# Optimization experiments

Hardware: AMD Instinct MI355X
Metric: run time of the kernel (lower is better)

Reference implementation:

```python
import jax, jax.numpy as jnp
import numpy as np

B, S, D, H = 8, 128, 256, 8
T = S + 1
HD = D // H  # head_dim = 32
GAMMA = 1.0
NEG_INF = -1e9
LN_EPS = 1e-5


def setup_inputs() -> dict:
    key = jax.random.key(0)
    ks = jax.random.split(key, 16)
    sc = 0.05
    return {
        "desc_embeddings": jax.random.normal(ks[0], (B, S, D), jnp.float32),
        "name_value_embeddings": jax.random.normal(ks[1], (B, T, D), jnp.float32),
        "prior_Q": jax.random.uniform(ks[2], (B, H, S, S), jnp.float32),
        "Wq": jax.random.normal(ks[3], (D, D), jnp.float32) * sc,
        "bq": jnp.zeros((D,), jnp.float32),
        "Wk": jax.random.normal(ks[4], (D, D), jnp.float32) * sc,
        "bk": jnp.zeros((D,), jnp.float32),
        "Wv": jax.random.normal(ks[5], (D, D), jnp.float32) * sc,
        "bv": jnp.zeros((D,), jnp.float32),
        "wa": jax.random.normal(ks[6], (3 * HD,), jnp.float32) * sc,  # attn_proj weight (out=1)
        "ba": jnp.zeros((), jnp.float32),
        "We1": jax.random.normal(ks[7], (2 * D, D), jnp.float32) * sc,
        "be1": jnp.zeros((D,), jnp.float32),
        "ln_g": jnp.ones((D,), jnp.float32),
        "ln_b": jnp.zeros((D,), jnp.float32),
        "We2": jax.random.normal(ks[8], (D, D), jnp.float32) * sc,
        "be2": jnp.zeros((D,), jnp.float32),
    }


def _layer_norm(x, g, b):
    mu = jnp.mean(x, axis=-1, keepdims=True)
    var = jnp.mean(jnp.square(x - mu), axis=-1, keepdims=True)
    return (x - mu) * jax.lax.rsqrt(var + LN_EPS) * g + b


def _heads(x, W, b):  # [B,T,D] -> [B,H,T,HD]
    return (x @ W + b).reshape(B, T, H, HD).transpose(0, 2, 1, 3)


def reference(desc_embeddings, name_value_embeddings, prior_Q,
              Wq, bq, Wk, bk, Wv, bv, wa, ba,
              We1, be1, ln_g, ln_b, We2, be2):
    # structural adjacency (same for every batch element): CLS->Var on, Var->CLS off,
    # Var-Var fully connected without self-loops
    adj = jnp.zeros((T, T), jnp.float32)
    adj = adj.at[1:, 1:].set(1.0 - jnp.eye(S, dtype=jnp.float32))
    adj = adj.at[0, 1:].set(1.0)

    q = _heads(name_value_embeddings, Wq, bq)  # [B,H,T,HD]
    k = _heads(name_value_embeddings, Wk, bk)
    v = _heads(name_value_embeddings, Wv, bv)

    # edge attributes: pairwise concat of desc embeddings, CLS rows/cols use [desc,desc]
    desc = desc_embeddings
    var_edge = jnp.concatenate([
        jnp.broadcast_to(desc[:, :, None, :], (B, S, S, D)),
        jnp.broadcast_to(desc[:, None, :, :], (B, S, S, D)),
    ], axis=-1)  # [B,S,S,2D]
    cls_edge = jnp.concatenate([desc, desc], axis=-1)  # [B,S,2D]
    edge = jnp.zeros((B, T, T, 2 * D), jnp.float32)
    edge = edge.at[:, 1:, 1:].set(var_edge)
    edge = edge.at[:, 0, 1:].set(cls_edge)
    edge = edge.at[:, 1:, 0].set(cls_edge)

    # edge_update MLP: Linear(2D->D) -> LayerNorm -> ReLU -> Linear(D->D)
    h = jax.nn.relu(_layer_norm(edge @ We1 + be1, ln_g, ln_b)) @ We2 + be2  # [B,T,T,D]
    # split into heads, mask by adjacency: [B,H,T,T,HD]
    edge_h = h.reshape(B, T, T, H, HD).transpose(0, 3, 1, 2, 4)
    edge_h = edge_h * adj[None, None, :, :, None]

    # gat_v1 + attn_proj(cat[q_i, k_j, e_ij]) is linear -> decompose to avoid
    # materializing the [B,H,T,T,3*HD] concat
    wa_q, wa_k, wa_e = wa[:HD], wa[HD:2 * HD], wa[2 * HD:]
    logits = (jnp.einsum('bhid,d->bhi', q, wa_q)[:, :, :, None]
              + jnp.einsum('bhjd,d->bhj', k, wa_k)[:, :, None, :]
              + jnp.einsum('bhijd,d->bhij', edge_h, wa_e)
              + ba)  # [B,H,T,T]

    # prior_Q logit-bias injection on Var-Var block
    eps = 1e-6
    p = jnp.clip(prior_Q, eps, 1.0 - eps)
    bias = (jnp.log(p) - jnp.log(1.0 - p)) * GAMMA  # [B,H,S,S]
    logits = logits.at[:, :, 1:, 1:].add(bias)

    # structural mask as pre-softmax -inf
    logits = logits + (adj == 0).astype(logits.dtype)[None, None] * NEG_INF

    attn = jax.nn.softmax(logits, axis=-1)  # [B,H,T,T]
    ctx = jnp.einsum('bhij,bhjd->bhid', attn, v)  # [B,H,T,HD]
    basis_outputs = ctx.transpose(0, 2, 1, 3)  # [B,T,H,HD]
    return basis_outputs, attn
```

## Files before the change

kernel.cpp:

```cpp
#include <hip/hip_runtime.h>
#include <math.h>

#define B 8
#define S 128
#define D 256
#define H 8
#define T 129
#define HD 32
#define NEG_INF -1000000000.0f
#define LN_EPS 1e-5f

__global__ __launch_bounds__(256) void gemm_all(
    const float* __restrict__ nv, const float* __restrict__ desc,
    const float* __restrict__ Wq, const float* __restrict__ bq,
    const float* __restrict__ Wk, const float* __restrict__ bk,
    const float* __restrict__ Wv, const float* __restrict__ bv,
    const float* __restrict__ We1, const float* __restrict__ be1,
    const float* __restrict__ We2, const float* __restrict__ be2,
    const float* __restrict__ wa,
    float* __restrict__ v, float* __restrict__ U, float* __restrict__ V,
    float* __restrict__ qdkd, float* __restrict__ W2aT, float* __restrict__ econst)
{
    const int blk = blockIdx.x;
    const int tid = threadIdx.x;

    __shared__ float xs[16][260];
    __shared__ float wq_s[256 * 16];
    __shared__ float bq_s[16];

    if (blk < 193) {
        const float* X; const float* W; const float* bias; float* out; int rows; int r0;
        if (blk < 65)       { X = nv;   W = Wv;        bias = bv;      out = v; rows = B*T; r0 = blk * 16; }
        else if (blk < 129) { X = desc; W = We1;       bias = be1;     out = U; rows = B*S; r0 = (blk - 65) * 16; }
        else                { X = desc; W = We1 + D*D; bias = nullptr; out = V; rows = B*S; r0 = (blk - 129) * 16; }

        for (int t = tid; t < 16 * 256; t += 256) {
            const int r = t >> 8, c = t & 255, rr = r0 + r;
            xs[r][c] = (rr < rows) ? X[rr * D + c] : 0.f;
        }
        __syncthreads();

        const int c  = tid & 127;
        const int rg = (tid >> 7) * 8;

        float acc[8][2];
        #pragma unroll
        for (int r = 0; r < 8; ++r) { acc[r][0] = 0.f; acc[r][1] = 0.f; }

        float wA[8], wB[8], nA[8], nB[8];
        #pragma unroll
        for (int q = 0; q < 8; ++q) { wA[q] = W[q*D + c]; wB[q] = W[q*D + c + 128]; }

        for (int kk = 0; kk < 256; kk += 8) {
            const int kn = kk + 8;
            if (kn < 256) {
                #pragma unroll
                for (int q = 0; q < 8; ++q) {
                    nA[q] = W[(kn + q)*D + c];
                    nB[q] = W[(kn + q)*D + c + 128];
                }
            }
            #pragma unroll
            for (int qh = 0; qh < 8; qh += 4) {
                #pragma unroll
                for (int r = 0; r < 8; ++r) {
                    const float4 x = *(const float4*)&xs[rg + r][kk + qh];
                    acc[r][0] = fmaf(x.x, wA[qh+0], acc[r][0]);
                    acc[r][0] = fmaf(x.y, wA[qh+1], acc[r][0]);
                    acc[r][0] = fmaf(x.z, wA[qh+2], acc[r][0]);
                    acc[r][0] = fmaf(x.w, wA[qh+3], acc[r][0]);
                    acc[r][1] = fmaf(x.x, wB[qh+0], acc[r][1]);
                    acc[r][1] = fmaf(x.y, wB[qh+1], acc[r][1]);
                    acc[r][1] = fmaf(x.z, wB[qh+2], acc[r][1]);
                    acc[r][1] = fmaf(x.w, wB[qh+3], acc[r][1]);
                }
            }
            if (kn < 256) {
                #pragma unroll
                for (int q = 0; q < 8; ++q) { wA[q] = nA[q]; wB[q] = nB[q]; }
            }
        }

        const float b0 = bias ? bias[c]       : 0.f;
        const float b1 = bias ? bias[c + 128] : 0.f;
        #pragma unroll
        for (int r = 0; r < 8; ++r) {
            const int rr = r0 + rg + r;
            if (rr < rows) {
                out[rr * D + c]       = acc[r][0] + b0;
                out[rr * D + c + 128] = acc[r][1] + b1;
            }
        }
    } else if (blk < 258) {
        const int r0 = (blk - 193) * 16;

        for (int t = tid; t < 4096; t += 256) {
            const int k = t >> 4, cc = t & 15;
            const float* Wsrc = (cc < 8) ? Wq : Wk;
            const float* wap  = (cc < 8) ? wa : wa + HD;
            const int h = cc & 7;
            float s = 0.f;
            #pragma unroll
            for (int d = 0; d < HD; ++d) s = fmaf(Wsrc[k*D + h*HD + d], wap[d], s);
            wq_s[t] = s;
        }
        if (tid < 16) {
            const float* bsrc = (tid < 8) ? bq : bk;
            const float* wap  = (tid < 8) ? wa : wa + HD;
            const int h = tid & 7;
            float s = 0.f;
            #pragma unroll
            for (int d = 0; d < HD; ++d) s = fmaf(bsrc[h*HD + d], wap[d], s);
            bq_s[tid] = s;
        }
        for (int t = tid; t < 16 * 256; t += 256) {
            const int r = t >> 8, c = t & 255, rr = r0 + r;
            xs[r][c] = (rr < B*T) ? nv[rr * D + c] : 0.f;
        }
        __syncthreads();

        const int r = tid >> 4, cc = tid & 15;
        float acc = 0.f;
        for (int kk = 0; kk < 256; kk += 4) {
            const float4 x = *(const float4*)&xs[r][kk];
            acc = fmaf(x.x, wq_s[(kk+0)*16 + cc], acc);
            acc = fmaf(x.y, wq_s[(kk+1)*16 + cc], acc);
            acc = fmaf(x.z, wq_s[(kk+2)*16 + cc], acc);
            acc = fmaf(x.w, wq_s[(kk+3)*16 + cc], acc);
        }
        const int rr = r0 + r;
        if (rr < B*T) qdkd[rr * 16 + cc] = acc + bq_s[cc];
    } else {
        for (int t = tid; t < 2048; t += 256) {
            const int h = t >> 8, c = t & 255;
            float s = 0.f;
            #pragma unroll
            for (int d = 0; d < HD; ++d) s = fmaf(We2[c*D + h*HD + d], wa[2*HD + d], s);
            W2aT[h*D + c] = s;
        }
        if (tid < 8) {
            float s = 0.f;
            #pragma unroll
            for (int d = 0; d < HD; ++d) s = fmaf(be2[tid*HD + d], wa[2*HD + d], s);
            econst[tid] = s;
        }
    }
}

__global__ __launch_bounds__(512) void edge_attn(
    const float* __restrict__ U, const float* __restrict__ V,
    const float* __restrict__ W2aT, const float* __restrict__ econst,
    const float* __restrict__ ln_g, const float* __restrict__ ln_b,
    const float* __restrict__ qdkd, const float* __restrict__ prior,
    const float* __restrict__ v, const float* __restrict__ ba,
    float* __restrict__ out_basis, float* __restrict__ out_attn)
{
    const int bid = blockIdx.x;
    const int b = bid / T, i = bid % T;
    const int tid = threadIdx.x, lane = tid & 63, wid = tid >> 6;
    const int c0 = lane * 4;

    __shared__ float escl[H][132];
    __shared__ float pat[H][132];

    const float4 g4 = *(const float4*)(ln_g + c0);
    const float4 b4 = *(const float4*)(ln_b + c0);
    float4 w[H];
    #pragma unroll
    for (int h = 0; h < H; ++h) w[h] = *(const float4*)(W2aT + h*D + c0);
    float4 u4i = make_float4(0.f, 0.f, 0.f, 0.f);
    if (i >= 1) u4i = *(const float4*)(U + (b*S + (i-1))*D + c0);

    const int hmap = 4*(lane&1) + 2*((lane>>1)&1) + ((lane>>2)&1);
    const float ecl = (lane < 8) ? econst[hmap] : 0.f;

    const int j0 = 1 + wid * 16;
    for (int jj = 0; jj < 16; ++jj) {
        const int j = j0 + jj;
        if (i >= 1 && j == i) continue;

        const float4 v4 = *(const float4*)(V + (b*S + (j-1))*D + c0);
        float4 u4;
        if (i == 0) u4 = *(const float4*)(U + (b*S + (j-1))*D + c0);
        else        u4 = u4i;

        const float y0 = u4.x + v4.x, y1 = u4.y + v4.y;
        const float y2 = u4.z + v4.z, y3 = u4.w + v4.w;

        float s1 = y0 + y1 + y2 + y3;
        float s2 = fmaf(y0, y0, fmaf(y1, y1, fmaf(y2, y2, y3 * y3)));
        #pragma unroll
        for (int m = 32; m >= 1; m >>= 1) {
            s1 += __shfl_xor(s1, m);
            s2 += __shfl_xor(s2, m);
        }
        const float mu  = s1 * (1.f / D);
        const float var = s2 * (1.f / D) - mu * mu;
        const float rs  = rsqrtf(var + LN_EPS);

        const float t0 = fmaxf((y0 - mu) * rs * g4.x + b4.x, 0.f);
        const float t1 = fmaxf((y1 - mu) * rs * g4.y + b4.y, 0.f);
        const float t2 = fmaxf((y2 - mu) * rs * g4.z + b4.z, 0.f);
        const float t3 = fmaxf((y3 - mu) * rs * g4.w + b4.w, 0.f);

        float ph[H];
        #pragma unroll
        for (int h = 0; h < H; ++h)
            ph[h] = fmaf(t0, w[h].x, fmaf(t1, w[h].y, fmaf(t2, w[h].z, t3 * w[h].w)));

        {
            const bool hi = (lane & 1);
            float k0 = hi ? ph[4] : ph[0], d0 = hi ? ph[0] : ph[4];
            float k1 = hi ? ph[5] : ph[1], d1 = hi ? ph[1] : ph[5];
            float k2 = hi ? ph[6] : ph[2], d2 = hi ? ph[2] : ph[6];
            float k3 = hi ? ph[7] : ph[3], d3 = hi ? ph[3] : ph[7];
            ph[0] = k0 + __shfl_xor(d0, 1);
            ph[1] = k1 + __shfl_xor(d1, 1);
            ph[2] = k2 + __shfl_xor(d2, 1);
            ph[3] = k3 + __shfl_xor(d3, 1);
        }
        {
            const bool hi = (lane & 2);
            float k0 = hi ? ph[2] : ph[0], d0 = hi ? ph[0] : ph[2];
            float k1 = hi ? ph[3] : ph[1], d1 = hi ? ph[1] : ph[3];
            ph[0] = k0 + __shfl_xor(d0, 2);
            ph[1] = k1 + __shfl_xor(d1, 2);
        }
        {
            const bool hi = (lane & 4);
            float k0 = hi ? ph[1] : ph[0], d0 = hi ? ph[0] : ph[1];
            ph[0] = k0 + __shfl_xor(d0, 4);
        }
        ph[0] += __shfl_xor(ph[0], 8);
        ph[0] += __shfl_xor(ph[0], 16);
        ph[0] += __shfl_xor(ph[0], 32);

        if (lane < 8) escl[hmap][j] = ph[0] + ecl;
    }
    __syncthreads();

    const int h = wid;
    const int bh = b*H + h;
    const float qdv = qdkd[(b*T + i)*16 + h];
    const float ba0 = ba[0];
    const int j1 = 1 + lane, j2 = 65 + lane;
    const bool v1 = !(i >= 1 && j1 == i);
    const bool v2 = !(i >= 1 && j2 == i);

    float l1 = NEG_INF, l2 = NEG_INF;
    if (v1) {
        l1 = qdv + qdkd[(b*T + j1)*16 + 8 + h] + escl[h][j1] + ba0;
        if (i >= 1) {
            float pr = prior[(bh*S + (i-1))*S + (j1-1)];
            pr = fminf(fmaxf(pr, 1e-6f), 1.f - 1e-6f);
            l1 += logf(pr) - logf(1.f - pr);
        }
    }
    if (v2) {
        l2 = qdv + qdkd[(b*T + j2)*16 + 8 + h] + escl[h][j2] + ba0;
        if (i >= 1) {
            float pr = prior[(bh*S + (i-1))*S + (j2-1)];
            pr = fminf(fmaxf(pr, 1e-6f), 1.f - 1e-6f);
            l2 += logf(pr) - logf(1.f - pr);
        }
    }

    float m = fmaxf(l1, l2);
    #pragma unroll
    for (int mm = 32; mm >= 1; mm >>= 1) m = fmaxf(m, __shfl_xor(m, mm));
    const float e1 = v1 ? expf(l1 - m) : 0.f;
    const float e2 = v2 ? expf(l2 - m) : 0.f;
    float s = e1 + e2;
    #pragma unroll
    for (int mm = 32; mm >= 1; mm >>= 1) s += __shfl_xor(s, mm);
    const float inv = 1.f / s;
    const float a1 = e1 * inv, a2 = e2 * inv;

    float* arow = out_attn + (size_t)(bh*T + i)*T;
    arow[j1] = a1;
    arow[j2] = a2;
    if (lane == 0) arow[0] = 0.f;
    pat[h][j1] = a1;
    pat[h][j2] = a2;
    __syncthreads();

    const int d = lane & 31, half = lane >> 5;
    float acc = 0.f;
    const float* vb = v + (size_t)(b*T)*D + h*HD + d;
    #pragma unroll 4
    for (int jj = 0; jj < 64; ++jj) {
        const int j = 1 + half*64 + jj;
        acc = fmaf(pat[h][j], vb[j*D], acc);
    }
    acc += __shfl_xor(acc, 32);
    if (lane < 32)
        out_basis[((b*T + i)*H + h)*HD + d] = acc;
}

extern "C" void kernel_launch(void* const* d_in, const int* in_sizes, int n_in,
                              void* d_out, int out_size, void* d_ws, size_t ws_size,
                              hipStream_t stream) {
    const float* desc  = (const float*)d_in[0];
    const float* nv    = (const float*)d_in[1];
    const float* prior = (const float*)d_in[2];
    const float* Wq  = (const float*)d_in[3];
    const float* bq  = (const float*)d_in[4];
    const float* Wk  = (const float*)d_in[5];
    const float* bk  = (const float*)d_in[6];
    const float* Wv  = (const float*)d_in[7];
    const float* bv  = (const float*)d_in[8];
    const float* wa  = (const float*)d_in[9];
    const float* ba  = (const float*)d_in[10];
    const float* We1 = (const float*)d_in[11];
    const float* be1 = (const float*)d_in[12];
    const float* lng = (const float*)d_in[13];
    const float* lnb = (const float*)d_in[14];
    const float* We2 = (const float*)d_in[15];
    const float* be2 = (const float*)d_in[16];

    float* ws = (float*)d_ws;
    float* U    = ws; ws += B*S*D;
    float* V    = ws; ws += B*S*D;
    float* v    = ws; ws += B*T*D;
    float* W2aT = ws; ws += H*D;
    float* ec   = ws; ws += H;
    float* qdkd = ws; ws += B*T*16;

    float* out_basis = (float*)d_out;
    float* out_attn  = out_basis + B*T*H*HD;

    gemm_all<<<dim3(259), 256, 0, stream>>>(nv, desc, Wq, bq, Wk, bk, Wv, bv,
                                            We1, be1, We2, be2, wa,
                                            v, U, V, qdkd, W2aT, ec);
    edge_attn<<<dim3(B*T), 512, 0, stream>>>(U, V, W2aT, ec, lng, lnb,
                                             qdkd, prior, v, ba,
                                             out_basis, out_attn);
}
```

Measured before the change: 178.0 us.

## Transpose edge projections and map one edge per thread in edge attention

The gemm stage now writes transposed copies of the U and V projections (feature-major per batch). It also uses smaller 4-row tiles that read inputs straight from global memory, which gives many more blocks. The edge kernel gives each thread one neighbor j and a 64-channel slice, with LayerNorm statistics and the per-head projections reduced through shared memory. This replaces the per-edge wavefront shuffle reductions. Fast-math exp/log intrinsics and explicit masking of the diagonal are added, at the cost of more shared memory, extra workspace and some loss of precision.

Measured after the change: 196.7 us. +10.5%, slower.

```diff
diff --git a/kernel.cpp b/kernel.cpp
--- a/kernel.cpp
+++ b/kernel.cpp
@@ -18,81 +18,85 @@
     const float* __restrict__ We1, const float* __restrict__ be1,
     const float* __restrict__ We2, const float* __restrict__ be2,
     const float* __restrict__ wa,
-    float* __restrict__ v, float* __restrict__ U, float* __restrict__ V,
-    float* __restrict__ qdkd, float* __restrict__ W2aT, float* __restrict__ econst)
+    float* __restrict__ v, float* __restrict__ U, float* __restrict__ Ut,
+    float* __restrict__ Vt, float* __restrict__ qdkd,
+    float* __restrict__ W2ca, float* __restrict__ econst)
 {
     const int blk = blockIdx.x;
     const int tid = threadIdx.x;
 
-    __shared__ float xs[16][260];
-    __shared__ float wq_s[256 * 16];
+    __shared__ float xs16[16 * 260];
+    __shared__ float wq_s[4096];
     __shared__ float bq_s[16];
 
-    if (blk < 193) {
-        const float* X; const float* W; const float* bias; float* out; int rows; int r0;
-        if (blk < 65)       { X = nv;   W = Wv;        bias = bv;      out = v; rows = B*T; r0 = blk * 16; }
-        else if (blk < 129) { X = desc; W = We1;       bias = be1;     out = U; rows = B*S; r0 = (blk - 65) * 16; }
-        else                { X = desc; W = We1 + D*D; bias = nullptr; out = V; rows = B*S; r0 = (blk - 129) * 16; }
-
-        for (int t = tid; t < 16 * 256; t += 256) {
-            const int r = t >> 8, c = t & 255, rr = r0 + r;
-            xs[r][c] = (rr < rows) ? X[rr * D + c] : 0.f;
-        }
-        __syncthreads();
-
-        const int c  = tid & 127;
-        const int rg = (tid >> 7) * 8;
-
-        float acc[8][2];
+    if (blk < 770) {
+        const float* X; const float* W; const float* bias; int r0; int mode;
+        if (blk < 258)      { X = nv;   W = Wv;        bias = bv;      r0 = blk * 4;         mode = 0; }
+        else if (blk < 514) { X = desc; W = We1;       bias = be1;     r0 = (blk - 258) * 4; mode = 1; }
+        else                { X = desc; W = We1 + D*D; bias = nullptr; r0 = (blk - 514) * 4; mode = 2; }
+        const int c = tid;
+
+        const float* x0 = X + (r0 + 0) * D;
+        const float* x1 = X + (r0 + 1) * D;
+        const float* x2 = X + (r0 + 2) * D;
+        const float* x3 = X + (r0 + 3) * D;
+
+        float acc0 = 0.f, acc1 = 0.f, acc2 = 0.f, acc3 = 0.f;
+        float w[8], nw[8];
         #pragma unroll
-        for (int r = 0; r < 8; ++r) { acc[r][0] = 0.f; acc[r][1] = 0.f; }
-
-        float wA[8], wB[8], nA[8], nB[8];
-        #pragma unroll
-        for (int q = 0; q < 8; ++q) { wA[q] = W[q*D + c]; wB[q] = W[q*D + c + 128]; }
+        for (int q = 0; q < 8; ++q) w[q] = W[q * D + c];
 
         for (int kk = 0; kk < 256; kk += 8) {
             const int kn = kk + 8;
             if (kn < 256) {
                 #pragma unroll
-                for (int q = 0; q < 8; ++q) {
-                    nA[q] = W[(kn + q)*D + c];
-                    nB[q] = W[(kn + q)*D + c + 128];
-                }
+                for (int q = 0; q < 8; ++q) nw[q] = W[(kn + q) * D + c];
             }
-            #pragma unroll
-            for (int qh = 0; qh < 8; qh += 4) {
-                #pragma unroll
-                for (int r = 0; r < 8; ++r) {
-                    const float4 x = *(const float4*)&xs[rg + r][kk + qh];
-                    acc[r][0] = fmaf(x.x, wA[qh+0], acc[r][0]);
-                    acc[r][0] = fmaf(x.y, wA[qh+1], acc[r][0]);
-                    acc[r][0] = fmaf(x.z, wA[qh+2], acc[r][0]);
-                    acc[r][0] = fmaf(x.w, wA[qh+3], acc[r][0]);
-                    acc[r][1] = fmaf(x.x, wB[qh+0], acc[r][1]);
-                    acc[r][1] = fmaf(x.y, wB[qh+1], acc[r][1]);
-                    acc[r][1] = fmaf(x.z, wB[qh+2], acc[r][1]);
-                    acc[r][1] = fmaf(x.w, wB[qh+3], acc[r][1]);
-                }
+            float xv0[8], xv1[8], xv2[8], xv3[8];
+            *(float4*)&xv0[0] = *(const float4*)(x0 + kk);
+            *(float4*)&xv0[4] = *(const float4*)(x0 + kk + 4);
+            *(float4*)&xv1[0] = *(const float4*)(x1 + kk);
+            *(float4*)&xv1[4] = *(const float4*)(x1 + kk + 4);
+            *(float4*)&xv2[0] = *(const float4*)(x2 + kk);
+            *(float4*)&xv2[4] = *(const float4*)(x2 + kk + 4);
+            *(float4*)&xv3[0] = *(const float4*)(x3 + kk);
+            *(float4*)&xv3[4] = *(const float4*)(x3 + kk + 4);
+            #pragma unroll
+            for (int q = 0; q < 8; ++q) {
+                acc0 = fmaf(xv0[q], w[q], acc0);
+                acc1 = fmaf(xv1[q], w[q], acc1);
+                acc2 = fmaf(xv2[q], w[q], acc2);
+                acc3 = fmaf(xv3[q], w[q], acc3);
             }
             if (kn < 256) {
                 #pragma unroll
-                for (int q = 0; q < 8; ++q) { wA[q] = nA[q]; wB[q] = nB[q]; }
+                for (int q = 0; q < 8; ++q) w[q] = nw[q];
             }
         }
 
-        const float b0 = bias ? bias[c]       : 0.f;
-        const float b1 = bias ? bias[c + 128] : 0.f;
-        #pragma unroll
-        for (int r = 0; r < 8; ++r) {
-            const int rr = r0 + rg + r;
-            if (rr < rows) {
-                out[rr * D + c]       = acc[r][0] + b0;
-                out[rr * D + c + 128] = acc[r][1] + b1;
+        const float bb = bias ? bias[c] : 0.f;
+        const float o0 = acc0 + bb, o1 = acc1 + bb, o2 = acc2 + bb, o3 = acc3 + bb;
+
+        if (mode == 0) {
+            v[(r0 + 0) * D + c] = o0;
+            v[(r0 + 1) * D + c] = o1;
+            v[(r0 + 2) * D + c] = o2;
+            v[(r0 + 3) * D + c] = o3;
+        } else {
+            const int b_ = r0 >> 7, rl = r0 & 127;
+            float4 tv; tv.x = o0; tv.y = o1; tv.z = o2; tv.w = o3;
+            if (mode == 1) {
+                U[(r0 + 0) * D + c] = o0;
+                U[(r0 + 1) * D + c] = o1;
+                U[(r0 + 2) * D + c] = o2;
+                U[(r0 + 3) * D + c] = o3;
+                *(float4*)&Ut[(b_ * D + c) * S + rl] = tv;
+            } else {
+                *(float4*)&Vt[(b_ * D + c) * S + rl] = tv;
             }
         }
-    } else if (blk < 258) {
-        const int r0 = (blk - 193) * 16;
+    } else if (blk < 835) {
+        const int r0 = (blk - 770) * 16;
 
         for (int t = tid; t < 4096; t += 256) {
             const int k = t >> 4, cc = t & 15;
@@ -114,15 +118,15 @@
             bq_s[tid] = s;
         }
         for (int t = tid; t < 16 * 256; t += 256) {
-            const int r = t >> 8, c = t & 255, rr = r0 + r;
-            xs[r][c] = (rr < B*T) ? nv[rr * D + c] : 0.f;
+            const int r = t >> 8, cch = t & 255, rr = r0 + r;
+            xs16[r * 260 + cch] = (rr < B*T) ? nv[rr * D + cch] : 0.f;
         }
         __syncthreads();
 
         const int r = tid >> 4, cc = tid & 15;
         float acc = 0.f;
         for (int kk = 0; kk < 256; kk += 4) {
-            const float4 x = *(const float4*)&xs[r][kk];
+            const float4 x = *(const float4*)&xs16[r * 260 + kk];
             acc = fmaf(x.x, wq_s[(kk+0)*16 + cc], acc);
             acc = fmaf(x.y, wq_s[(kk+1)*16 + cc], acc);
             acc = fmaf(x.z, wq_s[(kk+2)*16 + cc], acc);
@@ -132,11 +136,11 @@
         if (rr < B*T) qdkd[rr * 16 + cc] = acc + bq_s[cc];
     } else {
         for (int t = tid; t < 2048; t += 256) {
-            const int h = t >> 8, c = t & 255;
+            const int cch = t >> 3, h = t & 7;
             float s = 0.f;
             #pragma unroll
-            for (int d = 0; d < HD; ++d) s = fmaf(We2[c*D + h*HD + d], wa[2*HD + d], s);
-            W2aT[h*D + c] = s;
+            for (int d = 0; d < HD; ++d) s = fmaf(We2[cch*D + h*HD + d], wa[2*HD + d], s);
+            W2ca[t] = s;
         }
         if (tid < 8) {
             float s = 0.f;
@@ -148,8 +152,9 @@
 }
 
 __global__ __launch_bounds__(512) void edge_attn(
-    const float* __restrict__ U, const float* __restrict__ V,
-    const float* __restrict__ W2aT, const float* __restrict__ econst,
+    const float* __restrict__ U, const float* __restrict__ Ut,
+    const float* __restrict__ Vt,
+    const float* __restrict__ W2ca, const float* __restrict__ econst,
     const float* __restrict__ ln_g, const float* __restrict__ ln_b,
     const float* __restrict__ qdkd, const float* __restrict__ prior,
     const float* __restrict__ v, const float* __restrict__ ba,
@@ -158,143 +163,121 @@
     const int bid = blockIdx.x;
     const int b = bid / T, i = bid % T;
     const int tid = threadIdx.x, lane = tid & 63, wid = tid >> 6;
-    const int c0 = lane * 4;
-
-    __shared__ float escl[H][132];
-    __shared__ float pat[H][132];
-
-    const float4 g4 = *(const float4*)(ln_g + c0);
-    const float4 b4 = *(const float4*)(ln_b + c0);
-    float4 w[H];
-    #pragma unroll
-    for (int h = 0; h < H; ++h) w[h] = *(const float4*)(W2aT + h*D + c0);
-    float4 u4i = make_float4(0.f, 0.f, 0.f, 0.f);
-    if (i >= 1) u4i = *(const float4*)(U + (b*S + (i-1))*D + c0);
-
-    const int hmap = 4*(lane&1) + 2*((lane>>1)&1) + ((lane>>2)&1);
-    const float ecl = (lane < 8) ? econst[hmap] : 0.f;
-
-    const int j0 = 1 + wid * 16;
-    for (int jj = 0; jj < 16; ++jj) {
-        const int j = j0 + jj;
-        if (i >= 1 && j == i) continue;
-
-        const float4 v4 = *(const float4*)(V + (b*S + (j-1))*D + c0);
-        float4 u4;
-        if (i == 0) u4 = *(const float4*)(U + (b*S + (j-1))*D + c0);
-        else        u4 = u4i;
-
-        const float y0 = u4.x + v4.x, y1 = u4.y + v4.y;
-        const float y2 = u4.z + v4.z, y3 = u4.w + v4.w;
-
-        float s1 = y0 + y1 + y2 + y3;
-        float s2 = fmaf(y0, y0, fmaf(y1, y1, fmaf(y2, y2, y3 * y3)));
-        #pragma unroll
-        for (int m = 32; m >= 1; m >>= 1) {
-            s1 += __shfl_xor(s1, m);
-            s2 += __shfl_xor(s2, m);
-        }
-        const float mu  = s1 * (1.f / D);
-        const float var = s2 * (1.f / D) - mu * mu;
-        const float rs  = rsqrtf(var + LN_EPS);
-
-        const float t0 = fmaxf((y0 - mu) * rs * g4.x + b4.x, 0.f);
-        const float t1 = fmaxf((y1 - mu) * rs * g4.y + b4.y, 0.f);
-        const float t2 = fmaxf((y2 - mu) * rs * g4.z + b4.z, 0.f);
-        const float t3 = fmaxf((y3 - mu) * rs * g4.w + b4.w, 0.f);
-
-        float ph[H];
-        #pragma unroll
-        for (int h = 0; h < H; ++h)
-            ph[h] = fmaf(t0, w[h].x, fmaf(t1, w[h].y, fmaf(t2, w[h].z, t3 * w[h].w)));
-
-        {
-            const bool hi = (lane & 1);
-            float k0 = hi ? ph[4] : ph[0], d0 = hi ? ph[0] : ph[4];
-            float k1 = hi ? ph[5] : ph[1], d1 = hi ? ph[1] : ph[5];
-            float k2 = hi ? ph[6] : ph[2], d2 = hi ? ph[2] : ph[6];
-            float k3 = hi ? ph[7] : ph[3], d3 = hi ? ph[3] : ph[7];
-            ph[0] = k0 + __shfl_xor(d0, 1);
-            ph[1] = k1 + __shfl_xor(d1, 1);
-            ph[2] = k2 + __shfl_xor(d2, 1);
-            ph[3] = k3 + __shfl_xor(d3, 1);
-        }
-        {
-            const bool hi = (lane & 2);
-            float k0 = hi ? ph[2] : ph[0], d0 = hi ? ph[0] : ph[2];
-            float k1 = hi ? ph[3] : ph[1], d1 = hi ? ph[1] : ph[3];
-            ph[0] = k0 + __shfl_xor(d0, 2);
-            ph[1] = k1 + __shfl_xor(d1, 2);
-        }
-        {
-            const bool hi = (lane & 4);
-            float k0 = hi ? ph[1] : ph[0], d0 = hi ? ph[0] : ph[1];
-            ph[0] = k0 + __shfl_xor(d0, 4);
-        }
-        ph[0] += __shfl_xor(ph[0], 8);
-        ph[0] += __shfl_xor(ph[0], 16);
-        ph[0] += __shfl_xor(ph[0], 32);
-
-        if (lane < 8) escl[hmap][j] = ph[0] + ecl;
-    }
+    const int jh = wid & 1, cc = wid >> 1;
+    const int j = jh * 64 + lane;
+    const int cbase = cc * 64;
+
+    __shared__ float s1a[4][128], s2a[4][128];
+    __shared__ float part[4][8][128];
+    __shared__ float pat[8][128];
+
+    const float* vtb  = Vt + (size_t)b * D * S;
+    const float* utb  = Ut + (size_t)b * D * S;
+    const float* urow = U + (size_t)(b * S + (i >= 1 ? i - 1 : 0)) * D;
+
+    float s1 = 0.f, s2 = 0.f;
+    if (i >= 1) {
+        #pragma unroll 4
+        for (int c = cbase; c < cbase + 64; c += 4) {
+            const float4 u4 = *(const float4*)(urow + c);
+            const float v0 = vtb[(c+0)*S + j], v1 = vtb[(c+1)*S + j];
+            const float v2 = vtb[(c+2)*S + j], v3 = vtb[(c+3)*S + j];
+            const float y0 = u4.x + v0, y1 = u4.y + v1;
+            const float y2 = u4.z + v2, y3 = u4.w + v3;
+            s1 += y0 + y1 + y2 + y3;
+            s2 = fmaf(y0, y0, fmaf(y1, y1, fmaf(y2, y2, fmaf(y3, y3, s2))));
+        }
+    } else {
+        #pragma unroll 4
+        for (int c = cbase; c < cbase + 64; c += 4) {
+            const float y0 = utb[(c+0)*S + j] + vtb[(c+0)*S + j];
+            const float y1 = utb[(c+1)*S + j] + vtb[(c+1)*S + j];
+            const float y2 = utb[(c+2)*S + j] + vtb[(c+2)*S + j];
+            const float y3 = utb[(c+3)*S + j] + vtb[(c+3)*S + j];
+            s1 += y0 + y1 + y2 + y3;
+            s2 = fmaf(y0, y0, fmaf(y1, y1, fmaf(y2, y2, fmaf(y3, y3, s2))));
+        }
+    }
+    s1a[cc][j] = s1;
+    s2a[cc][j] = s2;
     __syncthreads();
 
+    const float st1 = s1a[0][j] + s1a[1][j] + s1a[2][j] + s1a[3][j];
+    const float st2 = s2a[0][j] + s2a[1][j] + s2a[2][j] + s2a[3][j];
+    const float mu  = st1 * (1.f / D);
+    const float var = st2 * (1.f / D) - mu * mu;
+    const float rs  = rsqrtf(var + LN_EPS);
+
+    float a0=0.f,a1=0.f,a2=0.f,a3=0.f,a4=0.f,a5=0.f,a6=0.f,a7=0.f;
+    #pragma unroll 4
+    for (int c = cbase; c < cbase + 64; ++c) {
+        const float u  = (i >= 1) ? urow[c] : utb[c*S + j];
+        const float vv = vtb[c*S + j];
+        float t = fmaf((u + vv - mu) * rs, ln_g[c], ln_b[c]);
+        t = fmaxf(t, 0.f);
+        const float4 wA = *(const float4*)(W2ca + c*8);
+        const float4 wB = *(const float4*)(W2ca + c*8 + 4);
+        a0 = fmaf(t, wA.x, a0); a1 = fmaf(t, wA.y, a1);
+        a2 = fmaf(t, wA.z, a2); a3 = fmaf(t, wA.w, a3);
+        a4 = fmaf(t, wB.x, a4); a5 = fmaf(t, wB.y, a5);
+        a6 = fmaf(t, wB.z, a6); a7 = fmaf(t, wB.w, a7);
+    }
+    part[cc][0][j] = a0; part[cc][1][j] = a1;
+    part[cc][2][j] = a2; part[cc][3][j] = a3;
+    part[cc][4][j] = a4; part[cc][5][j] = a5;
+    part[cc][6][j] = a6; part[cc][7][j] = a7;
+    __syncthreads();
+
     const int h = wid;
-    const int bh = b*H + h;
+    const float ecw = econst[h];
+    const float ba0 = ba[0];
     const float qdv = qdkd[(b*T + i)*16 + h];
-    const float ba0 = ba[0];
-    const int j1 = 1 + lane, j2 = 65 + lane;
-    const bool v1 = !(i >= 1 && j1 == i);
-    const bool v2 = !(i >= 1 && j2 == i);
-
-    float l1 = NEG_INF, l2 = NEG_INF;
-    if (v1) {
-        l1 = qdv + qdkd[(b*T + j1)*16 + 8 + h] + escl[h][j1] + ba0;
-        if (i >= 1) {
-            float pr = prior[(bh*S + (i-1))*S + (j1-1)];
-            pr = fminf(fmaxf(pr, 1e-6f), 1.f - 1e-6f);
-            l1 += logf(pr) - logf(1.f - pr);
-        }
-    }
-    if (v2) {
-        l2 = qdv + qdkd[(b*T + j2)*16 + 8 + h] + escl[h][j2] + ba0;
-        if (i >= 1) {
-            float pr = prior[(bh*S + (i-1))*S + (j2-1)];
-            pr = fminf(fmaxf(pr, 1e-6f), 1.f - 1e-6f);
-            l2 += logf(pr) - logf(1.f - pr);
-        }
+    const int j1 = lane, j2 = 64 + lane;
+
+    float e1s = part[0][h][j1] + part[1][h][j1] + part[2][h][j1] + part[3][h][j1];
+    float e2s = part[0][h][j2] + part[1][h][j2] + part[2][h][j2] + part[3][h][j2];
+    float l1 = qdv + qdkd[(b*T + 1 + j1)*16 + 8 + h] + e1s + ecw + ba0;
+    float l2 = qdv + qdkd[(b*T + 1 + j2)*16 + 8 + h] + e2s + ecw + ba0;
+    if (i >= 1) {
+        const float* prow = prior + ((size_t)(b*H + h)*S + (i-1))*S;
+        const float p1 = fminf(fmaxf(prow[j1], 1e-6f), 1.f - 1e-6f);
+        const float p2 = fminf(fmaxf(prow[j2], 1e-6f), 1.f - 1e-6f);
+        l1 += __logf(p1) - __logf(1.f - p1);
+        l2 += __logf(p2) - __logf(1.f - p2);
+        if (j1 == i - 1) l1 = NEG_INF;
+        if (j2 == i - 1) l2 = NEG_INF;
     }
 
     float m = fmaxf(l1, l2);
     #pragma unroll
     for (int mm = 32; mm >= 1; mm >>= 1) m = fmaxf(m, __shfl_xor(m, mm));
-    const float e1 = v1 ? expf(l1 - m) : 0.f;
-    const float e2 = v2 ? expf(l2 - m) : 0.f;
+    const float e1 = __expf(l1 - m);
+    const float e2 = __expf(l2 - m);
     float s = e1 + e2;
     #pragma unroll
     for (int mm = 32; mm >= 1; mm >>= 1) s += __shfl_xor(s, mm);
     const float inv = 1.f / s;
-    const float a1 = e1 * inv, a2 = e2 * inv;
-
-    float* arow = out_attn + (size_t)(bh*T + i)*T;
-    arow[j1] = a1;
-    arow[j2] = a2;
+    const float at1 = e1 * inv, at2 = e2 * inv;
+
+    float* arow = out_attn + (size_t)((b*H + h)*T + i)*T;
+    arow[1 + j1] = at1;
+    arow[1 + j2] = at2;
     if (lane == 0) arow[0] = 0.f;
-    pat[h][j1] = a1;
-    pat[h][j2] = a2;
+    pat[h][j1] = at1;
+    pat[h][j2] = at2;
     __syncthreads();
 
     const int d = lane & 31, half = lane >> 5;
     float acc = 0.f;
     const float* vb = v + (size_t)(b*T)*D + h*HD + d;
-    #pragma unroll 4
+    #pragma unroll 8
     for (int jj = 0; jj < 64; ++jj) {
-        const int j = 1 + half*64 + jj;
-        acc = fmaf(pat[h][j], vb[j*D], acc);
+        const int jc = half * 64 + jj;
+        acc = fmaf(pat[h][jc], vb[(size_t)(1 + jc)*D], acc);
     }
     acc += __shfl_xor(acc, 32);
     if (lane < 32)
-        out_basis[((b*T + i)*H + h)*HD + d] = acc;
+        out_basis[((size_t)(b*T + i)*H + h)*HD + d] = acc;
 }
 
 extern "C" void kernel_launch(void* const* d_in, const int* in_sizes, int n_in,
@@ -320,19 +303,20 @@
 
     float* ws = (float*)d_ws;
     float* U    = ws; ws += B*S*D;
-    float* V    = ws; ws += B*S*D;
+    float* Ut   = ws; ws += B*D*S;
+    float* Vt   = ws; ws += B*D*S;
     float* v    = ws; ws += B*T*D;
-    float* W2aT = ws; ws += H*D;
+    float* qdkd = ws; ws += B*T*16;
+    float* W2ca = ws; ws += D*H;
     float* ec   = ws; ws += H;
-    float* qdkd = ws; ws += B*T*16;
 
     float* out_basis = (float*)d_out;
     float* out_attn  = out_basis + B*T*H*HD;
 
-    gemm_all<<<dim3(259), 256, 0, stream>>>(nv, desc, Wq, bq, Wk, bk, Wv, bv,
+    gemm_all<<<dim3(836), 256, 0, stream>>>(nv, desc, Wq, bq, Wk, bk, Wv, bv,
                                             We1, be1, We2, be2, wa,
-                                            v, U, V, qdkd, W2aT, ec);
-    edge_attn<<<dim3(B*T), 512, 0, stream>>>(U, V, W2aT, ec, lng, lnb,
+                                            v, U, Ut, Vt, qdkd, W2ca, ec);
+    edge_attn<<<dim3(B*T), 512, 0, stream>>>(U, Ut, Vt, W2ca, ec, lng, lnb,
                                              qdkd, prior, v, ba,
                                              out_basis, out_attn);
 }
```

## Precompute LayerNorm stats algebraically via row sums and a U·V cross GEMM

Applied to the files above, without the earlier changes.

The per-edge LayerNorm mean and variance are now built from precomputed row sums and sums of squares of U and V, plus a cross term U_i·V_j. That cross term comes from a new small batched GEMM kernel that reads a transposed copy of V. This removes the per-edge wavefront shuffle reductions in edge_attn, at the cost of an extra launch, extra workspace, and a sum-of-squares variance formula that can lose precision. The projection GEMM is also restructured to 4 rows per block, reading activations straight from global memory. Exact log and exp are replaced by the fast __logf and __expf intrinsics.

Measured after the change: 179.8 us. About the same (+1.0%).

```diff
diff --git a/kernel.cpp b/kernel.cpp
--- a/kernel.cpp
+++ b/kernel.cpp
@@ -19,81 +19,112 @@
     const float* __restrict__ We2, const float* __restrict__ be2,
     const float* __restrict__ wa,
     float* __restrict__ v, float* __restrict__ U, float* __restrict__ V,
-    float* __restrict__ qdkd, float* __restrict__ W2aT, float* __restrict__ econst)
+    float* __restrict__ Vt, float* __restrict__ qdkd,
+    float* __restrict__ W2aT, float* __restrict__ econst,
+    float* __restrict__ sU, float* __restrict__ sU2,
+    float* __restrict__ sV, float* __restrict__ sV2)
 {
     const int blk = blockIdx.x;
     const int tid = threadIdx.x;
 
-    __shared__ float xs[16][260];
-    __shared__ float wq_s[256 * 16];
+    __shared__ float xs16[16 * 260];
+    __shared__ float wq_s[4096];
     __shared__ float bq_s[16];
-
-    if (blk < 193) {
-        const float* X; const float* W; const float* bias; float* out; int rows; int r0;
-        if (blk < 65)       { X = nv;   W = Wv;        bias = bv;      out = v; rows = B*T; r0 = blk * 16; }
-        else if (blk < 129) { X = desc; W = We1;       bias = be1;     out = U; rows = B*S; r0 = (blk - 65) * 16; }
-        else                { X = desc; W = We1 + D*D; bias = nullptr; out = V; rows = B*S; r0 = (blk - 129) * 16; }
-
-        for (int t = tid; t < 16 * 256; t += 256) {
-            const int r = t >> 8, c = t & 255, rr = r0 + r;
-            xs[r][c] = (rr < rows) ? X[rr * D + c] : 0.f;
-        }
-        __syncthreads();
-
-        const int c  = tid & 127;
-        const int rg = (tid >> 7) * 8;
-
-        float acc[8][2];
+    __shared__ float red[4][8];
+
+    if (blk < 770) {
+        const float* X; const float* W; const float* bias; int r0; int mode;
+        if (blk < 258)      { X = nv;   W = Wv;        bias = bv;      r0 = blk * 4;         mode = 0; }
+        else if (blk < 514) { X = desc; W = We1;       bias = be1;     r0 = (blk - 258) * 4; mode = 1; }
+        else                { X = desc; W = We1 + D*D; bias = nullptr; r0 = (blk - 514) * 4; mode = 2; }
+        const int c = tid;
+
+        const float* x0 = X + (r0 + 0) * D;
+        const float* x1 = X + (r0 + 1) * D;
+        const float* x2 = X + (r0 + 2) * D;
+        const float* x3 = X + (r0 + 3) * D;
+
+        float acc0 = 0.f, acc1 = 0.f, acc2 = 0.f, acc3 = 0.f;
+        float w[8], nw[8];
         #pragma unroll
-        for (int r = 0; r < 8; ++r) { acc[r][0] = 0.f; acc[r][1] = 0.f; }
-
-        float wA[8], wB[8], nA[8], nB[8];
-        #pragma unroll
-        for (int q = 0; q < 8; ++q) { wA[q] = W[q*D + c]; wB[q] = W[q*D + c + 128]; }
+        for (int q = 0; q < 8; ++q) w[q] = W[q * D + c];
 
         for (int kk = 0; kk < 256; kk += 8) {
             const int kn = kk + 8;
             if (kn < 256) {
                 #pragma unroll
-                for (int q = 0; q < 8; ++q) {
-                    nA[q] = W[(kn + q)*D + c];
-                    nB[q] = W[(kn + q)*D + c + 128];
-                }
-            }
-            #pragma unroll
-            for (int qh = 0; qh < 8; qh += 4) {
-                #pragma unroll
-                for (int r = 0; r < 8; ++r) {
-                    const float4 x = *(const float4*)&xs[rg + r][kk + qh];
-                    acc[r][0] = fmaf(x.x, wA[qh+0], acc[r][0]);
-                    acc[r][0] = fmaf(x.y, wA[qh+1], acc[r][0]);
-                    acc[r][0] = fmaf(x.z, wA[qh+2], acc[r][0]);
-                    acc[r][0] = fmaf(x.w, wA[qh+3], acc[r][0]);
-                    acc[r][1] = fmaf(x.x, wB[qh+0], acc[r][1]);
-                    acc[r][1] = fmaf(x.y, wB[qh+1], acc[r][1]);
-                    acc[r][1] = fmaf(x.z, wB[qh+2], acc[r][1]);
-                    acc[r][1] = fmaf(x.w, wB[qh+3], acc[r][1]);
-                }
+                for (int q = 0; q < 8; ++q) nw[q] = W[(kn + q) * D + c];
+            }
+            float xv0[8], xv1[8], xv2[8], xv3[8];
+            *(float4*)&xv0[0] = *(const float4*)(x0 + kk);
+            *(float4*)&xv0[4] = *(const float4*)(x0 + kk + 4);
+            *(float4*)&xv1[0] = *(const float4*)(x1 + kk);
+            *(float4*)&xv1[4] = *(const float4*)(x1 + kk + 4);
+            *(float4*)&xv2[0] = *(const float4*)(x2 + kk);
+            *(float4*)&xv2[4] = *(const float4*)(x2 + kk + 4);
+            *(float4*)&xv3[0] = *(const float4*)(x3 + kk);
+            *(float4*)&xv3[4] = *(const float4*)(x3 + kk + 4);
+            #pragma unroll
+            for (int q = 0; q < 8; ++q) {
+                acc0 = fmaf(xv0[q], w[q], acc0);
+                acc1 = fmaf(xv1[q], w[q], acc1);
+                acc2 = fmaf(xv2[q], w[q], acc2);
+                acc3 = fmaf(xv3[q], w[q], acc3);
             }
             if (kn < 256) {
                 #pragma unroll
-                for (int q = 0; q < 8; ++q) { wA[q] = nA[q]; wB[q] = nB[q]; }
-            }
-        }
-
-        const float b0 = bias ? bias[c]       : 0.f;
-        const float b1 = bias ? bias[c + 128] : 0.f;
-        #pragma unroll
-        for (int r = 0; r < 8; ++r) {
-            const int rr = r0 + rg + r;
-            if (rr < rows) {
-                out[rr * D + c]       = acc[r][0] + b0;
-                out[rr * D + c + 128] = acc[r][1] + b1;
-            }
-        }
-    } else if (blk < 258) {
-        const int r0 = (blk - 193) * 16;
-
+                for (int q = 0; q < 8; ++q) w[q] = nw[q];
+            }
+        }
+
+        const float bb = bias ? bias[c] : 0.f;
+        const float o0 = acc0 + bb, o1 = acc1 + bb, o2 = acc2 + bb, o3 = acc3 + bb;
+
+        if (mode == 0) {
+            if (r0 + 0 < B*T) v[(r0 + 0) * D + c] = o0;
+            if (r0 + 1 < B*T) v[(r0 + 1) * D + c] = o1;
+            if (r0 + 2 < B*T) v[(r0 + 2) * D + c] = o2;
+            if (r0 + 3 < B*T) v[(r0 + 3) * D + c] = o3;
+        } else {
+            if (mode == 1) {
+                U[(r0 + 0) * D + c] = o0;
+                U[(r0 + 1) * D + c] = o1;
+                U[(r0 + 2) * D + c] = o2;
+                U[(r0 + 3) * D + c] = o3;
+            } else {
+                V[(r0 + 0) * D + c] = o0;
+                V[(r0 + 1) * D + c] = o1;
+                V[(r0 + 2) * D + c] = o2;
+                V[(r0 + 3) * D + c] = o3;
+                const int b_ = r0 >> 7, rl = r0 & 127;
+                float4 tv; tv.x = o0; tv.y = o1; tv.z = o2; tv.w = o3;
+                *(float4*)&Vt[((size_t)b_ * D + c) * S + rl] = tv;
+            }
+            float s0 = o0, s1 = o1, s2 = o2, s3 = o3;
+            float q0 = o0*o0, q1 = o1*o1, q2 = o2*o2, q3 = o3*o3;
+            #pragma unroll
+            for (int m = 32; m >= 1; m >>= 1) {
+                s0 += __shfl_xor(s0, m); q0 += __shfl_xor(q0, m);
+                s1 += __shfl_xor(s1, m); q1 += __shfl_xor(q1, m);
+                s2 += __shfl_xor(s2, m); q2 += __shfl_xor(q2, m);
+                s3 += __shfl_xor(s3, m); q3 += __shfl_xor(q3, m);
+            }
+            const int wv = tid >> 6;
+            if ((tid & 63) == 0) {
+                red[wv][0] = s0; red[wv][1] = s1; red[wv][2] = s2; red[wv][3] = s3;
+                red[wv][4] = q0; red[wv][5] = q1; red[wv][6] = q2; red[wv][7] = q3;
+            }
+            __syncthreads();
+            if (tid < 4) {
+                const float ss = red[0][tid] + red[1][tid] + red[2][tid] + red[3][tid];
+                const float qq = red[0][4+tid] + red[1][4+tid] + red[2][4+tid] + red[3][4+tid];
+                const int row = r0 + tid;
+                if (mode == 1) { sU[row] = ss; sU2[row] = qq; }
+                else           { sV[row] = ss; sV2[row] = qq; }
+            }
+        }
+    } else if (blk < 835) {
+        const int r0 = (blk - 770) * 16;
         for (int t = tid; t < 4096; t += 256) {
             const int k = t >> 4, cc = t & 15;
             const float* Wsrc = (cc < 8) ? Wq : Wk;
@@ -114,15 +145,15 @@
             bq_s[tid] = s;
         }
         for (int t = tid; t < 16 * 256; t += 256) {
-            const int r = t >> 8, c = t & 255, rr = r0 + r;
-            xs[r][c] = (rr < B*T) ? nv[rr * D + c] : 0.f;
+            const int r = t >> 8, cch = t & 255, rr = r0 + r;
+            xs16[r * 260 + cch] = (rr < B*T) ? nv[rr * D + cch] : 0.f;
         }
         __syncthreads();
 
         const int r = tid >> 4, cc = tid & 15;
         float acc = 0.f;
         for (int kk = 0; kk < 256; kk += 4) {
-            const float4 x = *(const float4*)&xs[r][kk];
+            const float4 x = *(const float4*)&xs16[r * 260 + kk];
             acc = fmaf(x.x, wq_s[(kk+0)*16 + cc], acc);
             acc = fmaf(x.y, wq_s[(kk+1)*16 + cc], acc);
             acc = fmaf(x.z, wq_s[(kk+2)*16 + cc], acc);
@@ -132,11 +163,11 @@
         if (rr < B*T) qdkd[rr * 16 + cc] = acc + bq_s[cc];
     } else {
         for (int t = tid; t < 2048; t += 256) {
-            const int h = t >> 8, c = t & 255;
+            const int h = t >> 8, cch = t & 255;
             float s = 0.f;
             #pragma unroll
-            for (int d = 0; d < HD; ++d) s = fmaf(We2[c*D + h*HD + d], wa[2*HD + d], s);
-            W2aT[h*D + c] = s;
+            for (int d = 0; d < HD; ++d) s = fmaf(We2[cch*D + h*HD + d], wa[2*HD + d], s);
+            W2aT[h*D + cch] = s;
         }
         if (tid < 8) {
             float s = 0.f;
@@ -145,6 +176,31 @@
             econst[tid] = s;
         }
     }
+}
+
+__global__ __launch_bounds__(256) void uv_gemm(
+    const float* __restrict__ U, const float* __restrict__ Vt,
+    float* __restrict__ UV)
+{
+    const int br = blockIdx.x;
+    const int b  = br >> 7;
+    const int j  = threadIdx.x & 127, kh = threadIdx.x >> 7;
+    const float* urow = U + (size_t)br * D + kh * 128;
+    const float* vt   = Vt + (size_t)b * D * S + (size_t)kh * 128 * S;
+
+    float acc = 0.f;
+    #pragma unroll 8
+    for (int c = 0; c < 128; c += 4) {
+        const float4 u4 = *(const float4*)(urow + c);
+        acc = fmaf(u4.x, vt[(c+0)*S + j], acc);
+        acc = fmaf(u4.y, vt[(c+1)*S + j], acc);
+        acc = fmaf(u4.z, vt[(c+2)*S + j], acc);
+        acc = fmaf(u4.w, vt[(c+3)*S + j], acc);
+    }
+    __shared__ float part[2][128];
+    part[kh][j] = acc;
+    __syncthreads();
+    if (kh == 0) UV[(size_t)br * S + j] = part[0][j] + part[1][j];
 }
 
 __global__ __launch_bounds__(512) void edge_attn(
@@ -153,6 +209,9 @@
     const float* __restrict__ ln_g, const float* __restrict__ ln_b,
     const float* __restrict__ qdkd, const float* __restrict__ prior,
     const float* __restrict__ v, const float* __restrict__ ba,
+    const float* __restrict__ sU, const float* __restrict__ sU2,
+    const float* __restrict__ sV, const float* __restrict__ sV2,
+    const float* __restrict__ UV,
     float* __restrict__ out_basis, float* __restrict__ out_attn)
 {
     const int bid = blockIdx.x;
@@ -169,7 +228,14 @@
     #pragma unroll
     for (int h = 0; h < H; ++h) w[h] = *(const float4*)(W2aT + h*D + c0);
     float4 u4i = make_float4(0.f, 0.f, 0.f, 0.f);
-    if (i >= 1) u4i = *(const float4*)(U + (b*S + (i-1))*D + c0);
+    float su_i = 0.f, su2_i = 0.f;
+    const float* UVrow = UV;
+    if (i >= 1) {
+        u4i   = *(const float4*)(U + (size_t)(b*S + (i-1))*D + c0);
+        su_i  = sU [b*S + i-1];
+        su2_i = sU2[b*S + i-1];
+        UVrow = UV + (size_t)(b*S + (i-1))*S;
+    }
 
     const int hmap = 4*(lane&1) + 2*((lane>>1)&1) + ((lane>>2)&1);
     const float ecl = (lane < 8) ? econst[hmap] : 0.f;
@@ -179,24 +245,28 @@
         const int j = j0 + jj;
         if (i >= 1 && j == i) continue;
 
-        const float4 v4 = *(const float4*)(V + (b*S + (j-1))*D + c0);
+        const float svj  = sV [b*S + j-1];
+        const float sv2j = sV2[b*S + j-1];
+        float suv, su2v, cross;
+        if (i >= 1) {
+            suv = su_i; su2v = su2_i;
+            cross = UVrow[j-1];
+        } else {
+            suv   = sU [b*S + j-1];
+            su2v  = sU2[b*S + j-1];
+            cross = UV[(size_t)(b*S + j-1)*S + (j-1)];
+        }
+        const float mu  = (suv + svj) * (1.f / D);
+        const float ey2 = fmaf(2.f, cross, su2v + sv2j) * (1.f / D);
+        const float rs  = rsqrtf(ey2 - mu*mu + LN_EPS);
+
+        const float4 v4 = *(const float4*)(V + (size_t)(b*S + (j-1))*D + c0);
         float4 u4;
-        if (i == 0) u4 = *(const float4*)(U + (b*S + (j-1))*D + c0);
+        if (i == 0) u4 = *(const float4*)(U + (size_t)(b*S + (j-1))*D + c0);
         else        u4 = u4i;
 
         const float y0 = u4.x + v4.x, y1 = u4.y + v4.y;
         const float y2 = u4.z + v4.z, y3 = u4.w + v4.w;
-
-        float s1 = y0 + y1 + y2 + y3;
-        float s2 = fmaf(y0, y0, fmaf(y1, y1, fmaf(y2, y2, y3 * y3)));
-        #pragma unroll
-        for (int m = 32; m >= 1; m >>= 1) {
-            s1 += __shfl_xor(s1, m);
-            s2 += __shfl_xor(s2, m);
-        }
-        const float mu  = s1 * (1.f / D);
-        const float var = s2 * (1.f / D) - mu * mu;
-        const float rs  = rsqrtf(var + LN_EPS);
 
         const float t0 = fmaxf((y0 - mu) * rs * g4.x + b4.x, 0.f);
         const float t1 = fmaxf((y1 - mu) * rs * g4.y + b4.y, 0.f);
@@ -251,50 +321,50 @@
     if (v1) {
         l1 = qdv + qdkd[(b*T + j1)*16 + 8 + h] + escl[h][j1] + ba0;
         if (i >= 1) {
-            float pr = prior[(bh*S + (i-1))*S + (j1-1)];
+            float pr = prior[((size_t)bh*S + (i-1))*S + (j1-1)];
             pr = fminf(fmaxf(pr, 1e-6f), 1.f - 1e-6f);
-            l1 += logf(pr) - logf(1.f - pr);
+            l1 += __logf(pr) - __logf(1.f - pr);
         }
     }
     if (v2) {
         l2 = qdv + qdkd[(b*T + j2)*16 + 8 + h] + escl[h][j2] + ba0;
         if (i >= 1) {
-            float pr = prior[(bh*S + (i-1))*S + (j2-1)];
+            float pr = prior[((size_t)bh*S + (i-1))*S + (j2-1)];
             pr = fminf(fmaxf(pr, 1e-6f), 1.f - 1e-6f);
-            l2 += logf(pr) - logf(1.f - pr);
+            l2 += __logf(pr) - __logf(1.f - pr);
         }
     }
 
     float m = fmaxf(l1, l2);
     #pragma unroll
     for (int mm = 32; mm >= 1; mm >>= 1) m = fmaxf(m, __shfl_xor(m, mm));
-    const float e1 = v1 ? expf(l1 - m) : 0.f;
-    const float e2 = v2 ? expf(l2 - m) : 0.f;
+    const float e1 = v1 ? __expf(l1 - m) : 0.f;
+    const float e2 = v2 ? __expf(l2 - m) : 0.f;
     float s = e1 + e2;
     #pragma unroll
     for (int mm = 32; mm >= 1; mm >>= 1) s += __shfl_xor(s, mm);
     const float inv = 1.f / s;
-    const float a1 = e1 * inv, a2 = e2 * inv;
+    const float at1 = e1 * inv, at2 = e2 * inv;
 
     float* arow = out_attn + (size_t)(bh*T + i)*T;
-    arow[j1] = a1;
-    arow[j2] = a2;
+    arow[j1] = at1;
+    arow[j2] = at2;
     if (lane == 0) arow[0] = 0.f;
-    pat[h][j1] = a1;
-    pat[h][j2] = a2;
+    pat[h][j1] = at1;
+    pat[h][j2] = at2;
     __syncthreads();
 
     const int d = lane & 31, half = lane >> 5;
     float acc = 0.f;
     const float* vb = v + (size_t)(b*T)*D + h*HD + d;
-    #pragma unroll 4
+    #pragma unroll 8
     for (int jj = 0; jj < 64; ++jj) {
-        const int j = 1 + half*64 + jj;
-        acc = fmaf(pat[h][j], vb[j*D], acc);
+        const int jc = 1 + half*64 + jj;
+        acc = fmaf(pat[h][jc], vb[(size_t)jc * D], acc);
     }
     acc += __shfl_xor(acc, 32);
     if (lane < 32)
-        out_basis[((b*T + i)*H + h)*HD + d] = acc;
+        out_basis[((size_t)(b*T + i)*H + h)*HD + d] = acc;
 }
 
 extern "C" void kernel_launch(void* const* d_in, const int* in_sizes, int n_in,
@@ -321,18 +391,27 @@
     float* ws = (float*)d_ws;
     float* U    = ws; ws += B*S*D;
     float* V    = ws; ws += B*S*D;
+    float* Vt   = ws; ws += B*D*S;
     float* v    = ws; ws += B*T*D;
+    float* qdkd = ws; ws += B*T*16;
     float* W2aT = ws; ws += H*D;
     float* ec   = ws; ws += H;
-    float* qdkd = ws; ws += B*T*16;
+    float* sU   = ws; ws += B*S;
+    float* sU2  = ws; ws += B*S;
+    float* sV   = ws; ws += B*S;
+    float* sV2  = ws; ws += B*S;
+    float* UV   = ws; ws += B*S*S;
 
     float* out_basis = (float*)d_out;
     float* out_attn  = out_basis + B*T*H*HD;
 
-    gemm_all<<<dim3(259), 256, 0, stream>>>(nv, desc, Wq, bq, Wk, bk, Wv, bv,
+    gemm_all<<<dim3(836), 256, 0, stream>>>(nv, desc, Wq, bq, Wk, bk, Wv, bv,
                                             We1, be1, We2, be2, wa,
-                                            v, U, V, qdkd, W2aT, ec);
+                                            v, U, V, Vt, qdkd, W2aT, ec,
+                                            sU, sU2, sV, sV2);
+    uv_gemm<<<dim3(B*S), 256, 0, stream>>>(U, Vt, UV);
     edge_attn<<<dim3(B*T), 512, 0, stream>>>(U, V, W2aT, ec, lng, lnb,
                                              qdkd, prior, v, ba,
+                                             sU, sU2, sV, sV2, UV,
                                              out_basis, out_attn);
 }
```
